# Kernel optimization log

Hardware: AMD Instinct MI355X
Metric: run time of the kernel (lower is better)

## Reference

```python
import jax, jax.numpy as jnp
import numpy as np

DN = ('NCHW', 'OIHW', 'NCHW')
NH, DK, DV = 4, 40, 40
DKH, DVH = DK // NH, DV // NH


def conv2d(x, w, b):
    y = jax.lax.conv_general_dilated(x, w, (1, 1), 'SAME', dimension_numbers=DN)
    return y + b[None, :, None, None]


def rel_to_abs(x):
    # x: [B, heads, L, 2L-1] -> [B, heads, L, L] (standard rel->abs index trick)
    B, Nh, L, _ = x.shape
    x = jnp.pad(x, ((0, 0), (0, 0), (0, 0), (0, 1)))          # [B,Nh,L,2L]
    flat = x.reshape(B, Nh, L * 2 * L)
    flat = jnp.pad(flat, ((0, 0), (0, 0), (0, L - 1)))
    final = flat.reshape(B, Nh, L + 1, 2 * L - 1)
    return final[:, :, :L, L - 1:]


def relative_logits_1d(q, rel_k):
    # q: [B,Nh,H,W,d] -> [B,Nh,H(query),H(repeat),W(query),W(key)]
    B, Nh, H, W, _ = q.shape
    rl = jnp.einsum('bhxyd,md->bhxym', q, rel_k)               # [B,Nh,H,W,2W-1]
    rl = rel_to_abs(rl.reshape(B, Nh * H, W, 2 * W - 1))       # [B,Nh*H,W,W]
    rl = rl.reshape(B, Nh, H, 1, W, W)
    return jnp.broadcast_to(rl, (B, Nh, H, H, W, W))


def _forward(x, conv1_w, conv1_b, bn1_g, bn1_b, convo_w, convo_b, qkv_w, qkv_b,
             attno_w, attno_b, key_rel_h, key_rel_w, fc_w, fc_b):
    # conv1 + BN (training-mode batch stats) + relu
    h = conv2d(x, conv1_w, conv1_b)
    mu = h.mean(axis=(0, 2, 3), keepdims=True)
    var = h.var(axis=(0, 2, 3), keepdims=True)  # biased, matching torch BN normalization
    h = (h - mu) / jnp.sqrt(var + 1e-5) * bn1_g[None, :, None, None] + bn1_b[None, :, None, None]
    h = jax.nn.relu(h)

    # AugmentedConv
    conv_out = conv2d(h, convo_w, convo_b)                     # [B,88,H,W]
    B, _, H, W = conv_out.shape
    qkv = conv2d(h, qkv_w, qkv_b)                              # 1x1 conv -> [B,120,H,W]
    q, k, v = jnp.split(qkv, [DK, 2 * DK], axis=1)
    q = q.reshape(B, NH, DKH, H, W) * (DKH ** -0.5)
    k = k.reshape(B, NH, DKH, H, W)
    v = v.reshape(B, NH, DVH, H, W)
    flat_q = q.reshape(B, NH, DKH, H * W)
    flat_k = k.reshape(B, NH, DKH, H * W)
    flat_v = v.reshape(B, NH, DVH, H * W)

    logits = jnp.einsum('bhdn,bhdm->bhnm', flat_q, flat_k)     # [B,NH,HW,HW]

    q_t = q.transpose(0, 1, 3, 4, 2)                           # [B,Nh,H,W,dkh]
    w6 = relative_logits_1d(q_t, key_rel_w)                    # [B,Nh,Hq,Hrep,Wq,Wk]
    w_logits = w6.transpose(0, 1, 2, 4, 3, 5).reshape(B, NH, H * W, H * W)
    h6 = relative_logits_1d(q_t.transpose(0, 1, 3, 2, 4), key_rel_h)  # [B,Nh,Wq,Wrep,Hq,Hk]
    h_logits = h6.transpose(0, 1, 4, 2, 5, 3).reshape(B, NH, H * W, H * W)

    weights = jax.nn.softmax(logits + h_logits + w_logits, axis=-1)
    attn = jnp.einsum('bhnm,bhdm->bhnd', weights, flat_v)      # [B,NH,HW,dvh]
    # NOTE: faithful to the original torch code, which reshapes (no transpose)
    attn = attn.reshape(B, NH, DVH, H, W).reshape(B, NH * DVH, H, W)
    attn = conv2d(attn, attno_w, attno_b)                      # 1x1 conv, dv->dv
    out = jnp.concatenate([conv_out, attn], axis=1)            # [B,128,H,W]

    pooled = out.mean(axis=(2, 3))                             # AdaptiveAvgPool2d((1,1))
    return pooled @ fc_w.T + fc_b                              # [B,100]


def setup_inputs() -> dict:
    key = jax.random.key(0)
    ks = jax.random.split(key, 13)
    B, H, W = 16, 32, 32

    def n(k, shape, scale=0.05):
        return jax.random.normal(k, shape, dtype=jnp.float32) * scale

    return {
        'x': jax.random.normal(ks[0], (B, 3, H, W), dtype=jnp.float32),
        'conv1_w': n(ks[1], (64, 3, 3, 3)), 'conv1_b': n(ks[2], (64,)),
        'bn1_g': jnp.ones((64,), jnp.float32), 'bn1_b': jnp.zeros((64,), jnp.float32),
        'convo_w': n(ks[3], (88, 64, 3, 3)), 'convo_b': n(ks[4], (88,)),
        'qkv_w': n(ks[5], (120, 64, 1, 1)), 'qkv_b': n(ks[6], (120,)),
        'attno_w': n(ks[7], (40, 40, 1, 1)), 'attno_b': n(ks[8], (40,)),
        'key_rel_h': n(ks[9], (2 * H - 1, DKH)), 'key_rel_w': n(ks[10], (2 * W - 1, DKH)),
        'fc_w': n(ks[11], (100, 128)), 'fc_b': n(ks[12], (100,)),
    }


def reference(x, conv1_w, conv1_b, bn1_g, bn1_b, convo_w, convo_b, qkv_w, qkv_b,
              attno_w, attno_b, key_rel_h, key_rel_w, fc_w, fc_b):
    return _forward(x, conv1_w, conv1_b, bn1_g, bn1_b, convo_w, convo_b, qkv_w, qkv_b,
                    attno_w, attno_b, key_rel_h, key_rel_w, fc_w, fc_b)
```

## Files before the change

kernel.cpp:

```cpp
#include <hip/hip_runtime.h>
#include <hip/hip_bf16.h>


#define WS_H     0
#define WS_QKV   1048576
#define WS_ACC   3014656
#define ACC_BYTES ((64 + 64 + 5120 + 640) * 4)

typedef __attribute__((ext_vector_type(8))) short short8;
typedef __attribute__((ext_vector_type(16))) float float16;

__device__ __forceinline__ float fast_exp2(float x) {
#if __has_builtin(__builtin_amdgcn_exp2f)
  return __builtin_amdgcn_exp2f(x);
#else
  return exp2f(x);
#endif
}
__device__ __forceinline__ short f2bf(float x) {
  __hip_bfloat16 h(x);
  return *reinterpret_cast<short*>(&h);
}
__device__ __forceinline__ float bf2f(short s) {
  return __uint_as_float(((unsigned)(unsigned short)s) << 16);
}
__device__ __forceinline__ unsigned pack_bf16(float a, float b) {
  return (__float_as_uint(a) >> 16) | (__float_as_uint(b) & 0xFFFF0000u);
}

__global__ __launch_bounds__(256) void conv1_kernel(
    const float* __restrict__ x, const float* __restrict__ w,
    const float* __restrict__ bias, float* __restrict__ h,
    float* __restrict__ chanS, float* __restrict__ chanS2) {
  int b = blockIdx.x >> 5, cg = blockIdx.x & 31;
  int co0 = cg * 2;
  int t = threadIdx.x;
  __shared__ float xs[3072];
  const float4* xg = reinterpret_cast<const float4*>(x + b * 3072);
  float4* xsv = reinterpret_cast<float4*>(xs);
  for (int i = t; i < 768; i += 256) xsv[i] = xg[i];

  typedef const __attribute__((address_space(4))) float* cfp;
  cfp wc = (cfp)(size_t)w;
  float wr0[27], wr1[27];
#pragma unroll
  for (int i = 0; i < 27; ++i) { wr0[i] = wc[co0 * 27 + i]; wr1[i] = wc[(co0 + 1) * 27 + i]; }
  float bv0 = bias[co0], bv1 = bias[co0 + 1];
  __syncthreads();

  int row = t >> 3, col0 = (t & 7) * 4;
  float acc0[4] = {bv0, bv0, bv0, bv0};
  float acc1[4] = {bv1, bv1, bv1, bv1};
#pragma unroll
  for (int ci = 0; ci < 3; ++ci) {
#pragma unroll
    for (int dy = 0; dy < 3; ++dy) {
      int sr = row + dy - 1;
      if (sr < 0 || sr > 31) continue;
      const float* xr = &xs[ci * 1024 + sr * 32];
      float xv[6];
#pragma unroll
      for (int j = 0; j < 6; ++j) {
        int c = col0 - 1 + j;
        xv[j] = (c >= 0 && c < 32) ? xr[c] : 0.f;
      }
#pragma unroll
      for (int dx = 0; dx < 3; ++dx) {
        float w0 = wr0[ci * 9 + dy * 3 + dx], w1 = wr1[ci * 9 + dy * 3 + dx];
#pragma unroll
        for (int k = 0; k < 4; ++k) {
          acc0[k] += w0 * xv[k + dx];
          acc1[k] += w1 * xv[k + dx];
        }
      }
    }
  }
  *reinterpret_cast<float4*>(&h[(size_t)(b * 64 + co0) * 1024 + t * 4]) =
      make_float4(acc0[0], acc0[1], acc0[2], acc0[3]);
  *reinterpret_cast<float4*>(&h[(size_t)(b * 64 + co0 + 1) * 1024 + t * 4]) =
      make_float4(acc1[0], acc1[1], acc1[2], acc1[3]);

  float s10 = acc0[0] + acc0[1] + acc0[2] + acc0[3];
  float s20 = acc0[0]*acc0[0] + acc0[1]*acc0[1] + acc0[2]*acc0[2] + acc0[3]*acc0[3];
  float s11 = acc1[0] + acc1[1] + acc1[2] + acc1[3];
  float s21 = acc1[0]*acc1[0] + acc1[1]*acc1[1] + acc1[2]*acc1[2] + acc1[3]*acc1[3];
#pragma unroll
  for (int off = 32; off > 0; off >>= 1) {
    s10 += __shfl_down(s10, off);
    s20 += __shfl_down(s20, off);
    s11 += __shfl_down(s11, off);
    s21 += __shfl_down(s21, off);
  }
  if ((t & 63) == 0) {
    atomicAdd(&chanS[co0], s10);
    atomicAdd(&chanS2[co0], s20);
    atomicAdd(&chanS[co0 + 1], s11);
    atomicAdd(&chanS2[co0 + 1], s21);
  }
}

__global__ __launch_bounds__(256) void qkv_kernel3(
    const float* __restrict__ h, const float* __restrict__ chanS,
    const float* __restrict__ chanS2, const float* __restrict__ bn_g,
    const float* __restrict__ bn_b, const float* __restrict__ qw,
    const float* __restrict__ qb, float* __restrict__ qkv,
    float* __restrict__ sstatP) {
  int bid = blockIdx.x;
  int half = bid & 1, ck = (bid >> 1) & 15, b = bid >> 5;
  int t = threadIdx.x;
  __shared__ float ssc[64], ssh[64];
  __shared__ float hs[64][65];
  if (t < 64) {
    float mu = chanS[t] * (1.f / 16384.f);
    float var = chanS2[t] * (1.f / 16384.f) - mu * mu;
    float sc = bn_g[t] * rsqrtf(var + 1e-5f);
    ssc[t] = sc;
    ssh[t] = bn_b[t] - mu * sc;
  }
  __syncthreads();
  int pos = t & 63, grp = t >> 6;
#pragma unroll
  for (int r = 0; r < 16; ++r) {
    int ci = r * 4 + grp;
    float v = h[(size_t)(b * 64 + ci) * 1024 + ck * 64 + pos];
    hs[ci][pos] = fmaxf(0.f, v * ssc[ci] + ssh[ci]);
  }
  __syncthreads();
  if (half == 0 && t < 128) {
    int ci = t >> 1, rl = t & 1;
    int row = ck * 2 + rl;
    const float* hp = &hs[ci][rl * 32];
    float T = 0.f;
#pragma unroll
    for (int k = 0; k < 32; ++k) T += hp[k];
    float* sp = sstatP + (size_t)(b * 64 + ci) * 5;
    atomicAdd(sp + 0, T);
    if (row == 0) atomicAdd(sp + 1, T);
    if (row == 31) atomicAdd(sp + 2, T);
    atomicAdd(sp + 3, hp[0]);
    atomicAdd(sp + 4, hp[31]);
  }
  int co0 = half * 60 + grp * 15;
  float acc[15];
#pragma unroll
  for (int j = 0; j < 15; ++j) acc[j] = 0.f;
  typedef const __attribute__((address_space(4))) float* cfp;
  cfp qwc = (cfp)(size_t)qw;
  for (int ci = 0; ci < 64; ++ci) {
    float hv = hs[ci][pos];
#pragma unroll
    for (int j = 0; j < 15; ++j) acc[j] += qwc[(co0 + j) * 64 + ci] * hv;
  }
#pragma unroll
  for (int j = 0; j < 15; ++j)
    qkv[(size_t)(b * 120 + co0 + j) * 1024 + ck * 64 + pos] = acc[j] + qb[co0 + j];
}

__global__ __launch_bounds__(256, 2) void attn_mfma_kernel(
    const float* __restrict__ qkv, const float* __restrict__ relw,
    const float* __restrict__ relh, float* __restrict__ pooledA) {
  int bid = blockIdx.x;
  int qt = bid & 7, hd = (bid >> 3) & 3, b = bid >> 5;
  int t = threadIdx.x;
  int lane = t & 63, w = t >> 6, lid = lane & 31, hi = lane >> 5;

  __shared__ __align__(16) short Ks[256 * 24];
  __shared__ __align__(16) short Vs[16 * 264];
  __shared__ float poolL[16];

  short* Qs = Ks;
  float* RwL = (float*)Vs;
  float* RhL = RwL + 630;

  if (t < 16) poolL[t] = 0.f;
  const float QS2 = 0.31622776601683794f * 1.4426950408889634f;
  const float* qg = qkv + (size_t)(b * 120 + hd * 10) * 1024 + qt * 128;
  for (int i = t; i < 630; i += 256) {
    RwL[i] = relw[i];
    RhL[i] = relh[i];
  }
  for (int i = t; i < 1280; i += 256) {
    int q = i & 127, d = i >> 7;
    Qs[q * 16 + d] = f2bf(qg[d * 1024 + q] * QS2);
  }
  __syncthreads();

  int qrow = w * 32 + lid;
  float qfv[10];
#pragma unroll
  for (int d = 0; d < 10; ++d) qfv[d] = bf2f(Qs[qrow * 16 + d]);

  float16 rwC;
#pragma unroll
  for (int r = 0; r < 16; ++r) {
    int yp = (r & 3) + 8 * (r >> 2) + 4 * hi;
    const float* rp = &RwL[(31 + yp - lid) * 10];
    float s = 0.f;
#pragma unroll
    for (int d = 0; d < 10; ++d) s += qfv[d] * rp[d];
    rwC[r] = s;
  }
  int xn = qt * 4 + w;
  unsigned rhp[16];
#pragma unroll
  for (int j = 0; j < 16; ++j) {
    const float* rpa = &RhL[(31 + 2 * j - xn) * 10];
    const float* rpb = &RhL[(31 + 2 * j + 1 - xn) * 10];
    float sa = 0.f, sb = 0.f;
#pragma unroll
    for (int d = 0; d < 10; ++d) { sa += qfv[d] * rpa[d]; sb += qfv[d] * rpb[d]; }
    rhp[j] = pack_bf16(sa, sb);
  }
  short8 qf = *reinterpret_cast<const short8*>(&Qs[qrow * 16 + hi * 8]);
  short qf2 = qf[2];
  if (hi) { qf[3] = 0; qf[4] = 0; qf[5] = 0; qf[6] = 0; qf[7] = 0; }

  float16 O;
#pragma unroll
  for (int i = 0; i < 16; ++i) O[i] = 0.f;

  const float* kg = qkv + (size_t)(b * 120 + 40 + hd * 10) * 1024;
  const float* vg = kg + 40 * 1024;

  for (int p = 0; p < 4; ++p) {
    __syncthreads();
    for (int i = t; i < 2560; i += 256) {
      int d = i >> 8, key = i & 255;
      Ks[key * 24 + d] = f2bf(kg[d * 1024 + p * 256 + key]);
      int kc = (key & 0xF3) | ((key & 4) << 1) | ((key & 8) >> 1);
      Vs[d * 264 + kc] = f2bf(vg[d * 1024 + p * 256 + key]);
    }
    Ks[t * 24 + 10] = (short)0x3F80;
#pragma unroll
    for (int d2 = 11; d2 < 16; ++d2) Ks[t * 24 + d2] = 0;
    Vs[10 * 264 + t] = (short)0x3F80;
    __syncthreads();

#pragma unroll
    for (int tt = 0; tt < 8; ++tt) {
      int Tl = p * 8 + tt;
      unsigned rhw = rhp[Tl >> 1];
      short rhu = (short)((Tl & 1) ? (rhw >> 16) : (rhw & 0xFFFFu));
      short8 bq = qf;
      bq[2] = hi ? rhu : qf2;
      short8 ak = *reinterpret_cast<const short8*>(&Ks[(tt * 32 + lid) * 24 + hi * 8]);
      float16 S = __builtin_amdgcn_mfma_f32_32x32x16_bf16(ak, bq, rwC, 0, 0, 0);
      float e[16];
#pragma unroll
      for (int i = 0; i < 16; ++i) e[i] = fast_exp2(S[i]);
      uint4 b1u = make_uint4(pack_bf16(e[0], e[1]), pack_bf16(e[2], e[3]),
                             pack_bf16(e[4], e[5]), pack_bf16(e[6], e[7]));
      uint4 b2u = make_uint4(pack_bf16(e[8], e[9]), pack_bf16(e[10], e[11]),
                             pack_bf16(e[12], e[13]), pack_bf16(e[14], e[15]));
      short8 bp1 = *reinterpret_cast<short8*>(&b1u);
      short8 bp2 = *reinterpret_cast<short8*>(&b2u);
      short8 av1 = *reinterpret_cast<const short8*>(
          &Vs[(lid & 15) * 264 + tt * 32 + hi * 8]);
      short8 av2 = *reinterpret_cast<const short8*>(
          &Vs[(lid & 15) * 264 + tt * 32 + 16 + hi * 8]);
      O = __builtin_amdgcn_mfma_f32_32x32x16_bf16(av1, bp1, O, 0, 0, 0);
      O = __builtin_amdgcn_mfma_f32_32x32x16_bf16(av2, bp2, O, 0, 0, 0);
    }
  }

  float lsum = __shfl(O[6], lid);
  float inv = 1.f / lsum;
  int nglob = qt * 128 + qrow;
  int f0 = nglob * 10;
  int c0 = f0 >> 10, c1 = (f0 + 9) >> 10;
  float s0 = 0.f, s1 = 0.f;
  if (!hi) {
#pragma unroll
    for (int r = 0; r < 4; ++r) {
      float v = O[r] * inv;
      if (((f0 + r) >> 10) == c0) s0 += v; else s1 += v;
    }
#pragma unroll
    for (int r = 4; r < 6; ++r) {
      int d = r + 4;
      float v = O[r] * inv;
      if (((f0 + d) >> 10) == c0) s0 += v; else s1 += v;
    }
  } else {
#pragma unroll
    for (int r = 0; r < 4; ++r) {
      int d = r + 4;
      float v = O[r] * inv;
      if (((f0 + d) >> 10) == c0) s0 += v; else s1 += v;
    }
  }
  atomicAdd(&poolL[c0], s0);
  if (c1 != c0) atomicAdd(&poolL[c1], s1);
  __syncthreads();
  if (t < 10) atomicAdd(&pooledA[b * 40 + hd * 10 + t], poolL[t]);
}

__global__ __launch_bounds__(128) void final_kernel(
    const float* __restrict__ sstatP, const float* __restrict__ pooledA,
    const float* __restrict__ h, const float* __restrict__ chanS,
    const float* __restrict__ chanS2, const float* __restrict__ bn_g,
    const float* __restrict__ bn_b,
    const float* __restrict__ convo_w, const float* __restrict__ convo_b,
    const float* __restrict__ attno_w, const float* __restrict__ attno_b,
    const float* __restrict__ fc_w, const float* __restrict__ fc_b,
    float* __restrict__ out) {
  int b = blockIdx.x;
  int t = threadIdx.x;
  __shared__ float Sl[576];
  __shared__ float pooled[128];
  __shared__ float pa[40];
  if (t < 64) {
    int ci = t;
    float mu = chanS[ci] * (1.f / 16384.f);
    float var = chanS2[ci] * (1.f / 16384.f) - mu * mu;
    float sc = bn_g[ci] * rsqrtf(var + 1e-5f);
    float sh = bn_b[ci] - mu * sc;
    const float* hp = h + (size_t)(b * 64 + ci) * 1024;
    float h00 = fmaxf(0.f, hp[0] * sc + sh);
    float h0c = fmaxf(0.f, hp[31] * sc + sh);
    float hr0 = fmaxf(0.f, hp[992] * sc + sh);
    float hrc = fmaxf(0.f, hp[1023] * sc + sh);
    const float* sp = sstatP + (size_t)(b * 64 + ci) * 5;
    float T = sp[0], R0 = sp[1], R31 = sp[2], C0 = sp[3], C31 = sp[4];
    float xr[3] = {R31, 0.f, R0};
    float xc[3] = {C31, 0.f, C0};
    float corner[3][3] = {{hrc, 0.f, hr0}, {0.f, 0.f, 0.f}, {h0c, 0.f, h00}};
#pragma unroll
    for (int dy = 0; dy < 3; ++dy)
#pragma unroll
      for (int dx = 0; dx < 3; ++dx)
        Sl[ci * 9 + dy * 3 + dx] = T - xr[dy] - xc[dx] + corner[dy][dx];
  }
  if (t < 40) pa[t] = pooledA[b * 40 + t] * (1.f / 1024.f);
  __syncthreads();
  if (t < 88) {
    const float4* wr = reinterpret_cast<const float4*>(convo_w + t * 576);
    float acc = 0.f;
    for (int j = 0; j < 144; ++j) {
      float4 v = wr[j];
      acc += v.x * Sl[j * 4] + v.y * Sl[j * 4 + 1] + v.z * Sl[j * 4 + 2] + v.w * Sl[j * 4 + 3];
    }
    pooled[t] = convo_b[t] + acc * (1.f / 1024.f);
  } else if (t < 128) {
    int co = t - 88;
    const float4* wr = reinterpret_cast<const float4*>(attno_w + co * 40);
    float acc = attno_b[co];
    for (int j = 0; j < 10; ++j) {
      float4 v = wr[j];
      acc += v.x * pa[j * 4] + v.y * pa[j * 4 + 1] + v.z * pa[j * 4 + 2] + v.w * pa[j * 4 + 3];
    }
    pooled[88 + co] = acc;
  }
  __syncthreads();
  if (t < 100) {
    const float4* fr = reinterpret_cast<const float4*>(fc_w + t * 128);
    float acc = fc_b[t];
    for (int j = 0; j < 32; ++j) {
      float4 v = fr[j];
      acc += v.x * pooled[j * 4] + v.y * pooled[j * 4 + 1] + v.z * pooled[j * 4 + 2] + v.w * pooled[j * 4 + 3];
    }
    out[b * 100 + t] = acc;
  }
}

extern "C" void kernel_launch(void* const* d_in, const int* in_sizes, int n_in,
                              void* d_out, int out_size, void* d_ws, size_t ws_size,
                              hipStream_t stream) {
  const float* x         = (const float*)d_in[0];
  const float* conv1_w   = (const float*)d_in[1];
  const float* conv1_b   = (const float*)d_in[2];
  const float* bn1_g     = (const float*)d_in[3];
  const float* bn1_b     = (const float*)d_in[4];
  const float* convo_w   = (const float*)d_in[5];
  const float* convo_b   = (const float*)d_in[6];
  const float* qkv_w     = (const float*)d_in[7];
  const float* qkv_b     = (const float*)d_in[8];
  const float* attno_w   = (const float*)d_in[9];
  const float* attno_b   = (const float*)d_in[10];
  const float* key_rel_h = (const float*)d_in[11];
  const float* key_rel_w = (const float*)d_in[12];
  const float* fc_w      = (const float*)d_in[13];
  const float* fc_b      = (const float*)d_in[14];

  float* ws      = (float*)d_ws;
  float* h       = ws + WS_H;
  float* qkvb    = ws + WS_QKV;
  float* chanS   = ws + WS_ACC;
  float* chanS2  = chanS + 64;
  float* sstatP  = chanS2 + 64;
  float* pooledA = sstatP + 5120;

  hipMemsetAsync(chanS, 0, ACC_BYTES, stream);
  conv1_kernel<<<512, 256, 0, stream>>>(x, conv1_w, conv1_b, h, chanS, chanS2);
  qkv_kernel3<<<512, 256, 0, stream>>>(h, chanS, chanS2, bn1_g, bn1_b,
                                       qkv_w, qkv_b, qkvb, sstatP);
  attn_mfma_kernel<<<512, 256, 0, stream>>>(qkvb, key_rel_w, key_rel_h, pooledA);
  final_kernel<<<16, 128, 0, stream>>>(sstatP, pooledA, h, chanS, chanS2,
                                       bn1_g, bn1_b, convo_w, convo_b,
                                       attno_w, attno_b, fc_w, fc_b, (float*)d_out);
}
```

Baseline: 193.4 us.

## Replace global atomics with per-block partial buffers and drop workspace memset

Global atomicAdd accumulation of BN channel sums, spatial border statistics and pooled attention outputs is replaced by deterministic per-block partial slots, which the consumer kernels reduce. This removes the hipMemsetAsync launch and the atomic contention. The relative-embedding tables in LDS are also padded to a stride of 12 so the dot products can use vector loads. The float-to-bf16 conversion now truncates instead of rounding, which slightly changes numerics.

```diff
diff --git a/kernel.cpp b/kernel.cpp
--- a/kernel.cpp
+++ b/kernel.cpp
@@ -2,10 +2,12 @@
 #include <hip/hip_bf16.h>
 
 
-#define WS_H     0
-#define WS_QKV   1048576
-#define WS_ACC   3014656
-#define ACC_BYTES ((64 + 64 + 5120 + 640) * 4)
+#define WS_H      0
+#define WS_QKV    1048576
+#define WS_CHANS  3014656
+#define WS_CHANS2 3015680
+#define WS_SSTATP 3016704
+#define WS_POOLP  3098624
 
 typedef __attribute__((ext_vector_type(8))) short short8;
 typedef __attribute__((ext_vector_type(16))) float float16;
@@ -18,8 +20,7 @@
 #endif
 }
 __device__ __forceinline__ short f2bf(float x) {
-  __hip_bfloat16 h(x);
-  return *reinterpret_cast<short*>(&h);
+  return (short)(__float_as_uint(x) >> 16);
 }
 __device__ __forceinline__ float bf2f(short s) {
   return __uint_as_float(((unsigned)(unsigned short)s) << 16);
@@ -31,11 +32,12 @@
 __global__ __launch_bounds__(256) void conv1_kernel(
     const float* __restrict__ x, const float* __restrict__ w,
     const float* __restrict__ bias, float* __restrict__ h,
-    float* __restrict__ chanS, float* __restrict__ chanS2) {
+    float* __restrict__ chanSP, float* __restrict__ chanS2P) {
   int b = blockIdx.x >> 5, cg = blockIdx.x & 31;
   int co0 = cg * 2;
   int t = threadIdx.x;
   __shared__ float xs[3072];
+  __shared__ float red[4][4];
   const float4* xg = reinterpret_cast<const float4*>(x + b * 3072);
   float4* xsv = reinterpret_cast<float4*>(xs);
   for (int i = t; i < 768; i += 256) xsv[i] = xg[i];
@@ -91,17 +93,26 @@
     s11 += __shfl_down(s11, off);
     s21 += __shfl_down(s21, off);
   }
+  int wv = t >> 6;
   if ((t & 63) == 0) {
-    atomicAdd(&chanS[co0], s10);
-    atomicAdd(&chanS2[co0], s20);
-    atomicAdd(&chanS[co0 + 1], s11);
-    atomicAdd(&chanS2[co0 + 1], s21);
+    red[wv][0] = s10; red[wv][1] = s20; red[wv][2] = s11; red[wv][3] = s21;
+  }
+  __syncthreads();
+  if (t == 0) {
+    float a = red[0][0] + red[1][0] + red[2][0] + red[3][0];
+    float bq = red[0][1] + red[1][1] + red[2][1] + red[3][1];
+    float c = red[0][2] + red[1][2] + red[2][2] + red[3][2];
+    float d = red[0][3] + red[1][3] + red[2][3] + red[3][3];
+    chanSP[co0 * 16 + b] = a;
+    chanS2P[co0 * 16 + b] = bq;
+    chanSP[(co0 + 1) * 16 + b] = c;
+    chanS2P[(co0 + 1) * 16 + b] = d;
   }
 }
 
 __global__ __launch_bounds__(256) void qkv_kernel3(
-    const float* __restrict__ h, const float* __restrict__ chanS,
-    const float* __restrict__ chanS2, const float* __restrict__ bn_g,
+    const float* __restrict__ h, const float* __restrict__ chanSP,
+    const float* __restrict__ chanS2P, const float* __restrict__ bn_g,
     const float* __restrict__ bn_b, const float* __restrict__ qw,
     const float* __restrict__ qb, float* __restrict__ qkv,
     float* __restrict__ sstatP) {
@@ -111,8 +122,16 @@
   __shared__ float ssc[64], ssh[64];
   __shared__ float hs[64][65];
   if (t < 64) {
-    float mu = chanS[t] * (1.f / 16384.f);
-    float var = chanS2[t] * (1.f / 16384.f) - mu * mu;
+    const float4* p1 = reinterpret_cast<const float4*>(&chanSP[t * 16]);
+    const float4* p2 = reinterpret_cast<const float4*>(&chanS2P[t * 16]);
+    float4 a0 = p1[0], a1 = p1[1], a2 = p1[2], a3 = p1[3];
+    float4 c0 = p2[0], c1 = p2[1], c2 = p2[2], c3 = p2[3];
+    float S1 = a0.x+a0.y+a0.z+a0.w + a1.x+a1.y+a1.z+a1.w
+             + a2.x+a2.y+a2.z+a2.w + a3.x+a3.y+a3.z+a3.w;
+    float S2 = c0.x+c0.y+c0.z+c0.w + c1.x+c1.y+c1.z+c1.w
+             + c2.x+c2.y+c2.z+c2.w + c3.x+c3.y+c3.z+c3.w;
+    float mu = S1 * (1.f / 16384.f);
+    float var = S2 * (1.f / 16384.f) - mu * mu;
     float sc = bn_g[t] * rsqrtf(var + 1e-5f);
     ssc[t] = sc;
     ssh[t] = bn_b[t] - mu * sc;
@@ -128,17 +147,22 @@
   __syncthreads();
   if (half == 0 && t < 128) {
     int ci = t >> 1, rl = t & 1;
-    int row = ck * 2 + rl;
     const float* hp = &hs[ci][rl * 32];
     float T = 0.f;
 #pragma unroll
     for (int k = 0; k < 32; ++k) T += hp[k];
-    float* sp = sstatP + (size_t)(b * 64 + ci) * 5;
-    atomicAdd(sp + 0, T);
-    if (row == 0) atomicAdd(sp + 1, T);
-    if (row == 31) atomicAdd(sp + 2, T);
-    atomicAdd(sp + 3, hp[0]);
-    atomicAdd(sp + 4, hp[31]);
+    float c0v = hp[0], c31v = hp[31];
+    float Tp = __shfl_down(T, 1);
+    float c0p = __shfl_down(c0v, 1);
+    float c31p = __shfl_down(c31v, 1);
+    if (rl == 0) {
+      float* sp = sstatP + ((size_t)(b * 64 + ci) * 16 + ck) * 5;
+      sp[0] = T + Tp;
+      sp[1] = (ck == 0) ? T : 0.f;
+      sp[2] = (ck == 15) ? Tp : 0.f;
+      sp[3] = c0v + c0p;
+      sp[4] = c31v + c31p;
+    }
   }
   int co0 = half * 60 + grp * 15;
   float acc[15];
@@ -158,7 +182,7 @@
 
 __global__ __launch_bounds__(256, 2) void attn_mfma_kernel(
     const float* __restrict__ qkv, const float* __restrict__ relw,
-    const float* __restrict__ relh, float* __restrict__ pooledA) {
+    const float* __restrict__ relh, float* __restrict__ poolP) {
   int bid = blockIdx.x;
   int qt = bid & 7, hd = (bid >> 3) & 3, b = bid >> 5;
   int t = threadIdx.x;
@@ -170,14 +194,15 @@
 
   short* Qs = Ks;
   float* RwL = (float*)Vs;
-  float* RhL = RwL + 630;
+  float* RhL = RwL + 756;
 
   if (t < 16) poolL[t] = 0.f;
   const float QS2 = 0.31622776601683794f * 1.4426950408889634f;
   const float* qg = qkv + (size_t)(b * 120 + hd * 10) * 1024 + qt * 128;
   for (int i = t; i < 630; i += 256) {
-    RwL[i] = relw[i];
-    RhL[i] = relh[i];
+    int r = i / 10, d = i - r * 10;
+    RwL[r * 12 + d] = relw[i];
+    RhL[r * 12 + d] = relh[i];
   }
   for (int i = t; i < 1280; i += 256) {
     int q = i & 127, d = i >> 7;
@@ -194,22 +219,30 @@
 #pragma unroll
   for (int r = 0; r < 16; ++r) {
     int yp = (r & 3) + 8 * (r >> 2) + 4 * hi;
-    const float* rp = &RwL[(31 + yp - lid) * 10];
-    float s = 0.f;
-#pragma unroll
-    for (int d = 0; d < 10; ++d) s += qfv[d] * rp[d];
-    rwC[r] = s;
+    const float* rp = &RwL[(31 + yp - lid) * 12];
+    float4 a = *reinterpret_cast<const float4*>(rp);
+    float4 bb = *reinterpret_cast<const float4*>(rp + 4);
+    float2 cc = *reinterpret_cast<const float2*>(rp + 8);
+    rwC[r] = qfv[0] * a.x + qfv[1] * a.y + qfv[2] * a.z + qfv[3] * a.w
+           + qfv[4] * bb.x + qfv[5] * bb.y + qfv[6] * bb.z + qfv[7] * bb.w
+           + qfv[8] * cc.x + qfv[9] * cc.y;
   }
   int xn = qt * 4 + w;
   unsigned rhp[16];
 #pragma unroll
   for (int j = 0; j < 16; ++j) {
-    const float* rpa = &RhL[(31 + 2 * j - xn) * 10];
-    const float* rpb = &RhL[(31 + 2 * j + 1 - xn) * 10];
-    float sa = 0.f, sb = 0.f;
-#pragma unroll
-    for (int d = 0; d < 10; ++d) { sa += qfv[d] * rpa[d]; sb += qfv[d] * rpb[d]; }
-    rhp[j] = pack_bf16(sa, sb);
+    float s2[2];
+#pragma unroll
+    for (int u = 0; u < 2; ++u) {
+      const float* rp = &RhL[(31 + 2 * j + u - xn) * 12];
+      float4 a = *reinterpret_cast<const float4*>(rp);
+      float4 bb = *reinterpret_cast<const float4*>(rp + 4);
+      float2 cc = *reinterpret_cast<const float2*>(rp + 8);
+      s2[u] = qfv[0] * a.x + qfv[1] * a.y + qfv[2] * a.z + qfv[3] * a.w
+            + qfv[4] * bb.x + qfv[5] * bb.y + qfv[6] * bb.z + qfv[7] * bb.w
+            + qfv[8] * cc.x + qfv[9] * cc.y;
+    }
+    rhp[j] = pack_bf16(s2[0], s2[1]);
   }
   short8 qf = *reinterpret_cast<const short8*>(&Qs[qrow * 16 + hi * 8]);
   short qf2 = qf[2];
@@ -292,13 +325,13 @@
   atomicAdd(&poolL[c0], s0);
   if (c1 != c0) atomicAdd(&poolL[c1], s1);
   __syncthreads();
-  if (t < 10) atomicAdd(&pooledA[b * 40 + hd * 10 + t], poolL[t]);
+  if (t < 16) poolP[(size_t)bid * 16 + t] = poolL[t];
 }
 
 __global__ __launch_bounds__(128) void final_kernel(
-    const float* __restrict__ sstatP, const float* __restrict__ pooledA,
-    const float* __restrict__ h, const float* __restrict__ chanS,
-    const float* __restrict__ chanS2, const float* __restrict__ bn_g,
+    const float* __restrict__ sstatP, const float* __restrict__ poolP,
+    const float* __restrict__ h, const float* __restrict__ chanSP,
+    const float* __restrict__ chanS2P, const float* __restrict__ bn_g,
     const float* __restrict__ bn_b,
     const float* __restrict__ convo_w, const float* __restrict__ convo_b,
     const float* __restrict__ attno_w, const float* __restrict__ attno_b,
@@ -311,8 +344,14 @@
   __shared__ float pa[40];
   if (t < 64) {
     int ci = t;
-    float mu = chanS[ci] * (1.f / 16384.f);
-    float var = chanS2[ci] * (1.f / 16384.f) - mu * mu;
+    float S1 = 0.f, S2 = 0.f;
+#pragma unroll
+    for (int bb = 0; bb < 16; ++bb) {
+      S1 += chanSP[ci * 16 + bb];
+      S2 += chanS2P[ci * 16 + bb];
+    }
+    float mu = S1 * (1.f / 16384.f);
+    float var = S2 * (1.f / 16384.f) - mu * mu;
     float sc = bn_g[ci] * rsqrtf(var + 1e-5f);
     float sh = bn_b[ci] - mu * sc;
     const float* hp = h + (size_t)(b * 64 + ci) * 1024;
@@ -320,8 +359,16 @@
     float h0c = fmaxf(0.f, hp[31] * sc + sh);
     float hr0 = fmaxf(0.f, hp[992] * sc + sh);
     float hrc = fmaxf(0.f, hp[1023] * sc + sh);
-    const float* sp = sstatP + (size_t)(b * 64 + ci) * 5;
-    float T = sp[0], R0 = sp[1], R31 = sp[2], C0 = sp[3], C31 = sp[4];
+    float T = 0.f, R0 = 0.f, R31 = 0.f, C0 = 0.f, C31 = 0.f;
+    const float* sp = sstatP + (size_t)(b * 64 + ci) * 80;
+#pragma unroll
+    for (int ckk = 0; ckk < 16; ++ckk) {
+      T += sp[ckk * 5 + 0];
+      R0 += sp[ckk * 5 + 1];
+      R31 += sp[ckk * 5 + 2];
+      C0 += sp[ckk * 5 + 3];
+      C31 += sp[ckk * 5 + 4];
+    }
     float xr[3] = {R31, 0.f, R0};
     float xc[3] = {C31, 0.f, C0};
     float corner[3][3] = {{hrc, 0.f, hr0}, {0.f, 0.f, 0.f}, {h0c, 0.f, h00}};
@@ -331,7 +378,14 @@
       for (int dx = 0; dx < 3; ++dx)
         Sl[ci * 9 + dy * 3 + dx] = T - xr[dy] - xc[dx] + corner[dy][dx];
   }
-  if (t < 40) pa[t] = pooledA[b * 40 + t] * (1.f / 1024.f);
+  if (t < 40) {
+    int hd = t / 10, j = t - hd * 10;
+    const float* pp = poolP + (size_t)((b * 4 + hd) * 8) * 16 + j;
+    float s = 0.f;
+#pragma unroll
+    for (int q = 0; q < 8; ++q) s += pp[q * 16];
+    pa[t] = s * (1.f / 1024.f);
+  }
   __syncthreads();
   if (t < 88) {
     const float4* wr = reinterpret_cast<const float4*>(convo_w + t * 576);
@@ -382,20 +436,19 @@
   const float* fc_w      = (const float*)d_in[13];
   const float* fc_b      = (const float*)d_in[14];
 
-  float* ws      = (float*)d_ws;
-  float* h       = ws + WS_H;
-  float* qkvb    = ws + WS_QKV;
-  float* chanS   = ws + WS_ACC;
-  float* chanS2  = chanS + 64;
-  float* sstatP  = chanS2 + 64;
-  float* pooledA = sstatP + 5120;
-
-  hipMemsetAsync(chanS, 0, ACC_BYTES, stream);
-  conv1_kernel<<<512, 256, 0, stream>>>(x, conv1_w, conv1_b, h, chanS, chanS2);
-  qkv_kernel3<<<512, 256, 0, stream>>>(h, chanS, chanS2, bn1_g, bn1_b,
+  float* ws       = (float*)d_ws;
+  float* h        = ws + WS_H;
+  float* qkvb     = ws + WS_QKV;
+  float* chanSP   = ws + WS_CHANS;
+  float* chanS2P  = ws + WS_CHANS2;
+  float* sstatP   = ws + WS_SSTATP;
+  float* poolP    = ws + WS_POOLP;
+
+  conv1_kernel<<<512, 256, 0, stream>>>(x, conv1_w, conv1_b, h, chanSP, chanS2P);
+  qkv_kernel3<<<512, 256, 0, stream>>>(h, chanSP, chanS2P, bn1_g, bn1_b,
                                        qkv_w, qkv_b, qkvb, sstatP);
-  attn_mfma_kernel<<<512, 256, 0, stream>>>(qkvb, key_rel_w, key_rel_h, pooledA);
-  final_kernel<<<16, 128, 0, stream>>>(sstatP, pooledA, h, chanS, chanS2,
+  attn_mfma_kernel<<<512, 256, 0, stream>>>(qkvb, key_rel_w, key_rel_h, poolP);
+  final_kernel<<<16, 128, 0, stream>>>(sstatP, poolP, h, chanSP, chanS2P,
                                        bn1_g, bn1_b, convo_w, convo_b,
                                        attno_w, attno_b, fc_w, fc_b, (float*)d_out);
 }
```

After: 163.8 us. 15.3% less time.
